# Kernel optimization log

Measured on AMD Instinct MI355X. Metric: run time of the kernel, lower is better.

The kernel has to match this reference:

```python
import jax, jax.numpy as jnp
import numpy as np
from jax.scipy.special import logsumexp

EPSILON = 0.01        # temperature
DIST_THRESH = 0.2
NUM_ITERS = 3
NEG_INF = -1.0e9

B, N, M, C = 4, 4096, 4096, 256


def setup_inputs() -> dict:
    key = jax.random.key(0)
    k1, k2, k3, k4, k5 = jax.random.split(key, 5)
    source_feats = jax.random.normal(k1, (B, N, C), dtype=jnp.float32)
    source_locs = jax.random.uniform(k2, (B, N, 2), dtype=jnp.float32)
    target_locs = jax.random.uniform(k3, (B, M, 2), dtype=jnp.float32)
    source_valid_mask = jax.random.bernoulli(k4, 0.9, (B, N))
    target_valid_mask = jax.random.bernoulli(k5, 0.9, (B, M))
    return {
        "source_feats": source_feats,
        "source_locs": source_locs,
        "target_locs": target_locs,
        "source_valid_mask": source_valid_mask,
        "target_valid_mask": target_valid_mask,
    }


def reference(source_feats, source_locs, target_locs, source_valid_mask, target_valid_mask):
    # pairwise squared distances: [B, M, N]
    diff = target_locs[:, :, None, :] - source_locs[:, None, :, :]  # [B, M, N, 2]
    dist_sq = jnp.sum(diff * diff, axis=-1)                          # [B, M, N]
    log_K = -dist_sq / (EPSILON + 1e-8)

    valid_connection = dist_sq < (DIST_THRESH ** 2)
    valid_connection = valid_connection & source_valid_mask[:, None, :]
    valid_connection = valid_connection & target_valid_mask[:, :, None]
    log_K = jnp.where(valid_connection, log_K, NEG_INF)

    # Sinkhorn iterations in log space
    v = jnp.zeros((log_K.shape[0], 1, log_K.shape[2]), dtype=log_K.dtype)  # [B,1,N]
    u = jnp.zeros((log_K.shape[0], log_K.shape[1], 1), dtype=log_K.dtype)  # [B,M,1]
    for _ in range(NUM_ITERS):
        u = -logsumexp(log_K + v, axis=2, keepdims=True)
        v = -logsumexp(log_K + u, axis=1, keepdims=True)
        v = jnp.where(source_valid_mask[:, None, :], v, 0.0)

    attn = jnp.exp(log_K + u + v)  # [B, M, N]
    attn = jax.lax.stop_gradient(attn)  # original computes it under torch.no_grad

    target_feats = jnp.einsum('bmn,bnc->bmc', attn, source_feats)
    target_feats = target_feats * target_valid_mask[:, :, None].astype(target_feats.dtype)
    has_source = jnp.any(valid_connection, axis=-1, keepdims=True)
    target_feats = target_feats * has_source.astype(target_feats.dtype)
    return target_feats
```

## Files before the change

### kernel.cpp

```cpp
#include <hip/hip_runtime.h>
#include <math.h>

#define BB 4
#define BN 4096
#define CC 256
constexpr float T2      = 0.04f;
constexpr float NEGINF  = -1.0e9f;
constexpr float INV_EPS = (float)(1.0 / 0.01000001);

__device__ __forceinline__ int cell_of(float x, float y) {
  int cx = (int)(x * 5.0f); cx = cx < 0 ? 0 : (cx > 4 ? 4 : cx);
  int cy = (int)(y * 5.0f); cy = cy < 0 ? 0 : (cy > 4 ? 4 : cy);
  return cy * 5 + cx;
}

__global__ void k_count(const float* __restrict__ tlocs, const float* __restrict__ slocs,
                        int* __restrict__ counts_t, int* __restrict__ counts_s) {
  int gid = blockIdx.x * 256 + threadIdx.x;
  if (gid < BB * BN) {
    int b = gid >> 12;
    atomicAdd(&counts_t[b * 32 + cell_of(tlocs[gid * 2], tlocs[gid * 2 + 1])], 1);
  } else {
    int g = gid - BB * BN;
    int b = g >> 12;
    atomicAdd(&counts_s[b * 32 + cell_of(slocs[g * 2], slocs[g * 2 + 1])], 1);
  }
}

__global__ void k_scan_scatter(const float* __restrict__ tlocs, const float* __restrict__ slocs,
                               const int* __restrict__ tmask, const int* __restrict__ smask,
                               const int* __restrict__ counts_t, const int* __restrict__ counts_s,
                               int* __restrict__ starts_t, int* __restrict__ starts_s,
                               int* __restrict__ perm_t, int* __restrict__ perm_s,
                               float4* __restrict__ t_sorted, float4* __restrict__ s_sorted) {
  const int which = blockIdx.x & 1, b = blockIdx.x >> 1;
  const float* locs = which ? slocs : tlocs;
  const int*   mask = which ? smask : tmask;
  const int* counts = which ? counts_s : counts_t;
  int* starts       = which ? starts_s : starts_t;
  int* perm         = which ? perm_s : perm_t;
  float4* pack      = which ? s_sorted : t_sorted;
  __shared__ int st[26];
  __shared__ int cur[25];
  if (threadIdx.x == 0) {
    int acc = 0;
    for (int c = 0; c < 25; c++) { st[c] = acc; acc += counts[b * 32 + c]; }
    st[25] = acc;
  }
  __syncthreads();
  if (threadIdx.x < 25) cur[threadIdx.x] = st[threadIdx.x];
  if (threadIdx.x < 26) starts[b * 32 + threadIdx.x] = st[threadIdx.x];
  __syncthreads();
  for (int i = threadIdx.x; i < BN; i += 256) {
    float x = locs[(b * BN + i) * 2], y = locs[(b * BN + i) * 2 + 1];
    int pos = atomicAdd(&cur[cell_of(x, y)], 1);
    perm[b * BN + pos] = i;
    pack[b * BN + pos] = make_float4(x, y, 0.f, mask[b * BN + i] ? 1.f : 0.f);
  }
}

__global__ __launch_bounds__(256) void k_sink(const float4* __restrict__ opp,
                                              float4* __restrict__ own,
                                              const int* __restrict__ opp_starts,
                                              const int* __restrict__ Zin,
                                              int* __restrict__ Zout,
                                              int zero_invalid) {
  const int row  = blockIdx.x * 4 + (threadIdx.x >> 6);
  const int b    = row >> 12;
  const int lane = threadIdx.x & 63;
  const float4 me = own[row];
  float mrun = -1e30f, srun = 0.f;
  if (me.w != 0.f) {
    const int cell = cell_of(me.x, me.y);
    const int cy = cell / 5, cx = cell % 5;
    const int ry0 = max(cy - 1, 0), ry1 = min(cy + 1, 4);
    const int rx0 = max(cx - 1, 0), rx1 = min(cx + 1, 4);
    for (int ry = ry0; ry <= ry1; ry++) {
      const int r0 = opp_starts[b * 32 + ry * 5 + rx0];
      const int r1 = opp_starts[b * 32 + ry * 5 + rx1 + 1];
      for (int j = r0 + lane; j < r1; j += 64) {
        float4 o = opp[b * BN + j];
        float dx = me.x - o.x, dy = me.y - o.y;
        float d2 = fmaf(dx, dx, dy * dy);
        bool  c  = (d2 < T2) && (o.w != 0.f);
        float t  = c ? fmaf(d2, -INV_EPS, o.z) : -3e30f;
        float d  = t - mrun;
        float e  = __expf(-fabsf(d));
        if (d > 0.f) { srun = fmaf(srun, e, 1.f); mrun = t; }
        else         { srun += e; }
      }
    }
  }
  for (int off = 32; off > 0; off >>= 1) {
    float om = __shfl_down(mrun, off);
    float os = __shfl_down(srun, off);
    float nm = fmaxf(mrun, om);
    srun = srun * __expf(mrun - nm) + os * __expf(om - nm);
    mrun = nm;
  }
  if (lane == 0) {
    const int Z = Zin[b];
    float m0 = mrun, s = srun;
    if (Z > 0) {
      m0 = fmaxf(mrun, 0.f);
      s  = srun * __expf(mrun - m0) + (float)Z * __expf(-m0);
    }
    float val = (s > 0.f) ? -(m0 + logf(s)) : 1.0e9f;
    if (zero_invalid && me.w == 0.f) val = 0.f;
    own[row] = make_float4(me.x, me.y, val, me.w);
    if (val == 1.0e9f) atomicAdd(&Zout[b], 1);
  }
}

#define MAXCH 12

__global__ __launch_bounds__(256) void k_out(
    const float* __restrict__ feats, const float4* __restrict__ t_sorted,
    const float4* __restrict__ s_sorted, const int* __restrict__ perm_t,
    const int* __restrict__ perm_s, const int* __restrict__ starts_t,
    const int* __restrict__ starts_s, float* __restrict__ out) {
  const int b = blockIdx.z;
  const int cell = blockIdx.y / 3, rsel = blockIdx.y % 3;
  const int cy = cell / 5, cx = cell % 5;
  const int ry = cy + rsel - 1;
  if (ry < 0 || ry > 4) return;
  const int t0 = starts_t[b * 32 + cell], t1 = starts_t[b * 32 + cell + 1];
  const int base = t0 + blockIdx.x * 32;
  if (base >= t1) return;
  const int rx0 = max(cx - 1, 0), rx1 = min(cx + 1, 4);
  const int s0 = starts_s[b * 32 + ry * 5 + rx0];
  const int s1 = starts_s[b * 32 + ry * 5 + rx1 + 1];
  if (s0 >= s1) return;
  const int nt = min(32, t1 - base);

  __shared__ float4 tL[32];
  __shared__ int    morg[32];
  __shared__ float4 sL[16];
  __shared__ int    sorg[16];
  __shared__ __align__(16) float attnL[16][32];
  __shared__ __align__(16) float fL[16 * 256];

  const int tid = threadIdx.x;
  if (tid < 32) {
    if (tid < nt) {
      tL[tid]   = t_sorted[b * BN + base + tid];
      morg[tid] = perm_t[b * BN + base + tid];
    } else {
      tL[tid]   = make_float4(0.f, 0.f, 0.f, 0.f);
      morg[tid] = 0;
    }
  }
  const int tmg = tid >> 5;
  const int chg = tid & 31;
  float acc[4][8];
  #pragma unroll
  for (int i = 0; i < 4; i++)
    #pragma unroll
    for (int j = 0; j < 8; j++) acc[i][j] = 0.f;
  __syncthreads();

  for (int n0 = s0; n0 < s1; n0 += 16) {
    const int kk = min(16, s1 - n0);
    __syncthreads();
    if (tid < 16) {
      if (tid < kk) {
        sL[tid]   = s_sorted[b * BN + n0 + tid];
        sorg[tid] = perm_s[b * BN + n0 + tid];
      } else {
        sL[tid]   = make_float4(1e9f, 1e9f, 0.f, 0.f);
        sorg[tid] = 0;
      }
    }
    __syncthreads();
    {
      int e = tid * 2;
      #pragma unroll
      for (int q = 0; q < 2; q++, e++) {
        int nn = e >> 5, tm = e & 31;
        float4 t4 = tL[tm];
        float4 s4 = sL[nn];
        float dx = t4.x - s4.x, dy = t4.y - s4.y;
        float d2 = fmaf(dx, dx, dy * dy);
        bool  c  = (d2 < T2) && (s4.w != 0.f) && (t4.w != 0.f);
        attnL[nn][tm] = c ? __expf(fmaf(d2, -INV_EPS, t4.z + s4.z)) : 0.f;
      }
    }
    #pragma unroll
    for (int q = 0; q < 4; q++) {
      int idx = q * 256 + tid;
      ((float4*)fL)[idx] =
          ((const float4*)feats)[(((b << 12) + sorg[idx >> 6]) << 6) + (idx & 63)];
    }
    __syncthreads();
    #pragma unroll 4
    for (int nn = 0; nn < 16; nn++) {
      const float4 av = *(const float4*)&attnL[nn][tmg * 4];
      const float4 f0 = *(const float4*)&fL[nn * 256 + chg * 4];
      const float4 f1 = *(const float4*)&fL[nn * 256 + 128 + chg * 4];
      float avv[4] = {av.x, av.y, av.z, av.w};
      float ff[8]  = {f0.x, f0.y, f0.z, f0.w, f1.x, f1.y, f1.z, f1.w};
      #pragma unroll
      for (int i = 0; i < 4; i++)
        #pragma unroll
        for (int j = 0; j < 8; j++)
          acc[i][j] = fmaf(avv[i], ff[j], acc[i][j]);
    }
  }
  __syncthreads();
  #pragma unroll
  for (int i = 0; i < 4; i++) {
    int tm = tmg * 4 + i;
    if (tm < nt) {
      float* op = out + (((b << 12) + morg[tm]) << 8) + chg * 4;
      #pragma unroll
      for (int j = 0; j < 4; j++) atomicAdd(op + j,       acc[i][j]);
      #pragma unroll
      for (int j = 0; j < 4; j++) atomicAdd(op + 128 + j, acc[i][j + 4]);
    }
  }
}

extern "C" void kernel_launch(void* const* d_in, const int* in_sizes, int n_in,
                              void* d_out, int out_size, void* d_ws, size_t ws_size,
                              hipStream_t stream) {
  const float* feats = (const float*)d_in[0];
  const float* slocs = (const float*)d_in[1];
  const float* tlocs = (const float*)d_in[2];
  const int*   smask = (const int*)d_in[3];
  const int*   tmask = (const int*)d_in[4];
  float* out = (float*)d_out;

  char* ws = (char*)d_ws;
  int*    counts_t = (int*)(ws);
  int*    counts_s = (int*)(ws + 512);
  int*    Zc       = (int*)(ws + 1024);
  int*    starts_t = (int*)(ws + 2048);
  int*    starts_s = (int*)(ws + 2560);
  int*    perm_t   = (int*)(ws + 4096);
  int*    perm_s   = (int*)(ws + 69632);
  float4* s_sorted = (float4*)(ws + 135168);
  float4* t_sorted = (float4*)(ws + 397312);

  hipMemsetAsync(ws, 0, 2048, stream);
  hipMemsetAsync(out, 0, (size_t)out_size * sizeof(float), stream);
  k_count<<<128, 256, 0, stream>>>(tlocs, slocs, counts_t, counts_s);
  k_scan_scatter<<<8, 256, 0, stream>>>(tlocs, slocs, tmask, smask,
                                        counts_t, counts_s, starts_t, starts_s,
                                        perm_t, perm_s, t_sorted, s_sorted);
  for (int it = 0; it < 3; it++) {
    k_sink<<<4096, 256, 0, stream>>>(s_sorted, t_sorted, starts_s,
                                     Zc + (it == 0 ? 0 : (2 * it) * 4),
                                     Zc + (2 * it + 1) * 4, 0);
    k_sink<<<4096, 256, 0, stream>>>(t_sorted, s_sorted, starts_t,
                                     Zc + (2 * it + 1) * 4,
                                     Zc + (2 * it + 2) * 4, 1);
  }
  k_out<<<dim3(MAXCH, 75, BB), 256, 0, stream>>>(feats, t_sorted, s_sorted,
                                                 perm_t, perm_s, starts_t,
                                                 starts_s, out);
}
```

Before: 604.0 us.

## Fuse Sinkhorn passes into cooperative kernel and drop atomics in output kernel

The six per-half-iteration Sinkhorn launches become one cooperative kernel that loops over phases with grid-wide syncs, removing five launch gaps. The output kernel now lets each block walk all three neighbouring source row bands itself. Each block owns a 128-channel half for its 32 targets, so results are written with plain float4 stores instead of atomics, and the output memset goes away. Source features and attention tiles are double-buffered through registers and shared memory to overlap global loads with the multiply-accumulate. The costs are a reliance on cooperative launch residency (1024 blocks), grid.sync overhead, and serialising over more source chunks per block.

```diff
diff --git a/kernel.cpp b/kernel.cpp
--- a/kernel.cpp
+++ b/kernel.cpp
@@ -1,11 +1,12 @@
 #include <hip/hip_runtime.h>
+#include <hip/hip_cooperative_groups.h>
 #include <math.h>
+
+namespace cg = cooperative_groups;
 
 #define BB 4
 #define BN 4096
-#define CC 256
 constexpr float T2      = 0.04f;
-constexpr float NEGINF  = -1.0e9f;
 constexpr float INV_EPS = (float)(1.0 / 0.01000001);
 
 __device__ __forceinline__ int cell_of(float x, float y) {
@@ -59,88 +60,108 @@
   }
 }
 
-__global__ __launch_bounds__(256) void k_sink(const float4* __restrict__ opp,
-                                              float4* __restrict__ own,
-                                              const int* __restrict__ opp_starts,
-                                              const int* __restrict__ Zin,
-                                              int* __restrict__ Zout,
-                                              int zero_invalid) {
-  const int row  = blockIdx.x * 4 + (threadIdx.x >> 6);
-  const int b    = row >> 12;
+__global__ __launch_bounds__(256) void k_sink_all(
+    float4* __restrict__ t_sorted, float4* __restrict__ s_sorted,
+    const int* __restrict__ starts_t, const int* __restrict__ starts_s,
+    int* __restrict__ Zc) {
+  cg::grid_group grid = cg::this_grid();
+  const int wid  = (blockIdx.x << 2) + (threadIdx.x >> 6);
   const int lane = threadIdx.x & 63;
-  const float4 me = own[row];
-  float mrun = -1e30f, srun = 0.f;
-  if (me.w != 0.f) {
-    const int cell = cell_of(me.x, me.y);
-    const int cy = cell / 5, cx = cell % 5;
-    const int ry0 = max(cy - 1, 0), ry1 = min(cy + 1, 4);
-    const int rx0 = max(cx - 1, 0), rx1 = min(cx + 1, 4);
-    for (int ry = ry0; ry <= ry1; ry++) {
-      const int r0 = opp_starts[b * 32 + ry * 5 + rx0];
-      const int r1 = opp_starts[b * 32 + ry * 5 + rx1 + 1];
-      for (int j = r0 + lane; j < r1; j += 64) {
-        float4 o = opp[b * BN + j];
-        float dx = me.x - o.x, dy = me.y - o.y;
-        float d2 = fmaf(dx, dx, dy * dy);
-        bool  c  = (d2 < T2) && (o.w != 0.f);
-        float t  = c ? fmaf(d2, -INV_EPS, o.z) : -3e30f;
-        float d  = t - mrun;
-        float e  = __expf(-fabsf(d));
-        if (d > 0.f) { srun = fmaf(srun, e, 1.f); mrun = t; }
-        else         { srun += e; }
-      }
-    }
-  }
-  for (int off = 32; off > 0; off >>= 1) {
-    float om = __shfl_down(mrun, off);
-    float os = __shfl_down(srun, off);
-    float nm = fmaxf(mrun, om);
-    srun = srun * __expf(mrun - nm) + os * __expf(om - nm);
-    mrun = nm;
-  }
-  if (lane == 0) {
-    const int Z = Zin[b];
-    float m0 = mrun, s = srun;
-    if (Z > 0) {
-      m0 = fmaxf(mrun, 0.f);
-      s  = srun * __expf(mrun - m0) + (float)Z * __expf(-m0);
-    }
-    float val = (s > 0.f) ? -(m0 + logf(s)) : 1.0e9f;
-    if (zero_invalid && me.w == 0.f) val = 0.f;
-    own[row] = make_float4(me.x, me.y, val, me.w);
-    if (val == 1.0e9f) atomicAdd(&Zout[b], 1);
+  for (int ph = 0; ph < 6; ph++) {
+    float4*       own = (ph & 1) ? s_sorted : t_sorted;
+    const float4* opp = (ph & 1) ? t_sorted : s_sorted;
+    const int*    ost = (ph & 1) ? starts_t : starts_s;
+    const int* Zin = Zc + ph * 4;
+    int*      Zout = Zc + (ph + 1) * 4;
+    const int zero_invalid = (ph & 1);
+    for (int row = wid; row < BB * BN; row += 4096) {
+      const int b = row >> 12;
+      const float4 me = own[row];
+      float mrun = -1e30f, srun = 0.f;
+      if (me.w != 0.f) {
+        const int cell = cell_of(me.x, me.y);
+        const int cy = cell / 5, cx = cell % 5;
+        const int ry0 = max(cy - 1, 0), ry1 = min(cy + 1, 4);
+        const int rx0 = max(cx - 1, 0), rx1 = min(cx + 1, 4);
+        for (int ry = ry0; ry <= ry1; ry++) {
+          const int r0 = ost[b * 32 + ry * 5 + rx0];
+          const int r1 = ost[b * 32 + ry * 5 + rx1 + 1];
+          for (int j = r0 + lane; j < r1; j += 64) {
+            float4 o = opp[b * BN + j];
+            float dx = me.x - o.x, dy = me.y - o.y;
+            float d2 = fmaf(dx, dx, dy * dy);
+            bool  c  = (d2 < T2) && (o.w != 0.f);
+            float t  = c ? fmaf(d2, -INV_EPS, o.z) : -3e30f;
+            float d  = t - mrun;
+            float e  = __expf(-fabsf(d));
+            if (d > 0.f) { srun = fmaf(srun, e, 1.f); mrun = t; }
+            else         { srun += e; }
+          }
+        }
+      }
+      for (int off = 32; off > 0; off >>= 1) {
+        float om = __shfl_down(mrun, off);
+        float os = __shfl_down(srun, off);
+        float nm = fmaxf(mrun, om);
+        srun = srun * __expf(mrun - nm) + os * __expf(om - nm);
+        mrun = nm;
+      }
+      if (lane == 0) {
+        const int Z = Zin[b];
+        float m0 = mrun, s = srun;
+        if (Z > 0) {
+          m0 = fmaxf(mrun, 0.f);
+          s  = srun * __expf(mrun - m0) + (float)Z * __expf(-m0);
+        }
+        float val = (s > 0.f) ? -(m0 + logf(s)) : 1.0e9f;
+        if (zero_invalid && me.w == 0.f) val = 0.f;
+        own[row] = make_float4(me.x, me.y, val, me.w);
+        if (val == 1.0e9f) atomicAdd(&Zout[b], 1);
+      }
+    }
+    grid.sync();
   }
 }
 
 #define MAXCH 12
 
 __global__ __launch_bounds__(256) void k_out(
-    const float* __restrict__ feats, const float4* __restrict__ t_sorted,
+    const float4* __restrict__ featsF4, const float4* __restrict__ t_sorted,
     const float4* __restrict__ s_sorted, const int* __restrict__ perm_t,
     const int* __restrict__ perm_s, const int* __restrict__ starts_t,
-    const int* __restrict__ starts_s, float* __restrict__ out) {
-  const int b = blockIdx.z;
-  const int cell = blockIdx.y / 3, rsel = blockIdx.y % 3;
-  const int cy = cell / 5, cx = cell % 5;
-  const int ry = cy + rsel - 1;
-  if (ry < 0 || ry > 4) return;
+    const int* __restrict__ starts_s, float4* __restrict__ outF4) {
+  const int b    = blockIdx.z >> 1;
+  const int chO  = (blockIdx.z & 1) << 5;
+  const int cell = blockIdx.y;
   const int t0 = starts_t[b * 32 + cell], t1 = starts_t[b * 32 + cell + 1];
   const int base = t0 + blockIdx.x * 32;
   if (base >= t1) return;
+  const int nt = min(32, t1 - base);
+
+  const int cy = cell / 5, cx = cell % 5;
   const int rx0 = max(cx - 1, 0), rx1 = min(cx + 1, 4);
-  const int s0 = starts_s[b * 32 + ry * 5 + rx0];
-  const int s1 = starts_s[b * 32 + ry * 5 + rx1 + 1];
-  if (s0 >= s1) return;
-  const int nt = min(32, t1 - base);
+  int r0[3], len[3];
+  #pragma unroll
+  for (int k = 0; k < 3; k++) {
+    int ry = cy + k - 1;
+    if (ry >= 0 && ry <= 4) {
+      int a = starts_s[b * 32 + ry * 5 + rx0];
+      int e = starts_s[b * 32 + ry * 5 + rx1 + 1];
+      r0[k] = a; len[k] = e - a;
+    } else { r0[k] = 0; len[k] = 0; }
+  }
+  const int total   = len[0] + len[1] + len[2];
+  const int nchunks = (total + 15) >> 4;
 
   __shared__ float4 tL[32];
   __shared__ int    morg[32];
-  __shared__ float4 sL[16];
-  __shared__ int    sorg[16];
-  __shared__ __align__(16) float attnL[16][32];
-  __shared__ __align__(16) float fL[16 * 256];
-
-  const int tid = threadIdx.x;
+  __shared__ __align__(16) float  attnL[2][16][32];
+  __shared__ __align__(16) float4 fL[2][512];
+
+  const int tid  = threadIdx.x;
+  const int w    = tid >> 6, lane = tid & 63;
+  const int tmg  = tid >> 5, chg = tid & 31;
+
   if (tid < 32) {
     if (tid < nt) {
       tL[tid]   = t_sorted[b * BN + base + tid];
@@ -150,72 +171,112 @@
       morg[tid] = 0;
     }
   }
-  const int tmg = tid >> 5;
-  const int chg = tid & 31;
-  float acc[4][8];
+
+  float acc[4][4];
   #pragma unroll
   for (int i = 0; i < 4; i++)
     #pragma unroll
-    for (int j = 0; j < 8; j++) acc[i][j] = 0.f;
+    for (int j = 0; j < 4; j++) acc[i][j] = 0.f;
+
+  float4 sreg = make_float4(1e9f, 1e9f, 0.f, 0.f);
+  int    sorgreg = 0;
+  auto loadS = [&](int chunk) {
+    int v  = chunk * 16 + lane;
+    int jj = -1;
+    if (v < len[0]) jj = r0[0] + v;
+    else {
+      v -= len[0];
+      if (v < len[1]) jj = r0[1] + v;
+      else {
+        v -= len[1];
+        if (v < len[2]) jj = r0[2] + v;
+      }
+    }
+    if (lane < 16) {
+      if (jj >= 0) {
+        sreg    = s_sorted[b * BN + jj];
+        sorgreg = perm_s[b * BN + jj];
+      } else {
+        sreg    = make_float4(1e9f, 1e9f, 0.f, 0.f);
+        sorgreg = 0;
+      }
+    }
+  };
+  float4 greg[2];
+  auto issue_loads = [&]() {
+    #pragma unroll
+    for (int q = 0; q < 2; q++) {
+      int row = (w << 2) + (q << 1) + (lane >> 5);
+      int so  = __shfl(sorgreg, row);
+      greg[q] = featsF4[(((b << 12) + so) << 6) + chO + (lane & 31)];
+    }
+  };
+  auto write_fl = [&](int bi) {
+    #pragma unroll
+    for (int q = 0; q < 2; q++)
+      fL[bi][(w << 7) + (q << 6) + lane] = greg[q];
+  };
+  auto stage_attn = [&](int bi) {
+    #pragma unroll
+    for (int q = 0; q < 2; q++) {
+      int e  = tid * 2 + q;
+      int nn = e >> 5, tm = e & 31;
+      float sx = __shfl(sreg.x, nn);
+      float sy = __shfl(sreg.y, nn);
+      float sv = __shfl(sreg.z, nn);
+      float sw = __shfl(sreg.w, nn);
+      float4 t4 = tL[tm];
+      float dx = t4.x - sx, dy = t4.y - sy;
+      float d2 = fmaf(dx, dx, dy * dy);
+      bool  c  = (d2 < T2) && (sw != 0.f) && (t4.w != 0.f);
+      attnL[bi][nn][tm] = c ? __expf(fmaf(d2, -INV_EPS, t4.z + sv)) : 0.f;
+    }
+  };
+  auto mac = [&](int bi) {
+    #pragma unroll
+    for (int nn = 0; nn < 16; nn++) {
+      const float4 av = *(const float4*)&attnL[bi][nn][tmg << 2];
+      const float4 f  = fL[bi][(nn << 5) + chg];
+      #pragma unroll
+      for (int i = 0; i < 4; i++) {
+        float a = (&av.x)[i];
+        acc[i][0] = fmaf(a, f.x, acc[i][0]);
+        acc[i][1] = fmaf(a, f.y, acc[i][1]);
+        acc[i][2] = fmaf(a, f.z, acc[i][2]);
+        acc[i][3] = fmaf(a, f.w, acc[i][3]);
+      }
+    }
+  };
+
+  loadS(0);
   __syncthreads();
-
-  for (int n0 = s0; n0 < s1; n0 += 16) {
-    const int kk = min(16, s1 - n0);
+  if (nchunks > 0) {
+    issue_loads();
+    write_fl(0);
+    stage_attn(0);
+    loadS(1);
+  }
+  __syncthreads();
+
+  for (int i = 0; i < nchunks; i++) {
+    const int cur = i & 1, nxt = cur ^ 1;
+    const bool more = (i + 1) < nchunks;
+    if (more) issue_loads();
+    mac(cur);
+    if (more) {
+      write_fl(nxt);
+      stage_attn(nxt);
+      loadS(i + 2);
+    }
     __syncthreads();
-    if (tid < 16) {
-      if (tid < kk) {
-        sL[tid]   = s_sorted[b * BN + n0 + tid];
-        sorg[tid] = perm_s[b * BN + n0 + tid];
-      } else {
-        sL[tid]   = make_float4(1e9f, 1e9f, 0.f, 0.f);
-        sorg[tid] = 0;
-      }
-    }
-    __syncthreads();
-    {
-      int e = tid * 2;
-      #pragma unroll
-      for (int q = 0; q < 2; q++, e++) {
-        int nn = e >> 5, tm = e & 31;
-        float4 t4 = tL[tm];
-        float4 s4 = sL[nn];
-        float dx = t4.x - s4.x, dy = t4.y - s4.y;
-        float d2 = fmaf(dx, dx, dy * dy);
-        bool  c  = (d2 < T2) && (s4.w != 0.f) && (t4.w != 0.f);
-        attnL[nn][tm] = c ? __expf(fmaf(d2, -INV_EPS, t4.z + s4.z)) : 0.f;
-      }
-    }
-    #pragma unroll
-    for (int q = 0; q < 4; q++) {
-      int idx = q * 256 + tid;
-      ((float4*)fL)[idx] =
-          ((const float4*)feats)[(((b << 12) + sorg[idx >> 6]) << 6) + (idx & 63)];
-    }
-    __syncthreads();
-    #pragma unroll 4
-    for (int nn = 0; nn < 16; nn++) {
-      const float4 av = *(const float4*)&attnL[nn][tmg * 4];
-      const float4 f0 = *(const float4*)&fL[nn * 256 + chg * 4];
-      const float4 f1 = *(const float4*)&fL[nn * 256 + 128 + chg * 4];
-      float avv[4] = {av.x, av.y, av.z, av.w};
-      float ff[8]  = {f0.x, f0.y, f0.z, f0.w, f1.x, f1.y, f1.z, f1.w};
-      #pragma unroll
-      for (int i = 0; i < 4; i++)
-        #pragma unroll
-        for (int j = 0; j < 8; j++)
-          acc[i][j] = fmaf(avv[i], ff[j], acc[i][j]);
-    }
-  }
-  __syncthreads();
+  }
+
   #pragma unroll
   for (int i = 0; i < 4; i++) {
-    int tm = tmg * 4 + i;
+    int tm = (tmg << 2) + i;
     if (tm < nt) {
-      float* op = out + (((b << 12) + morg[tm]) << 8) + chg * 4;
-      #pragma unroll
-      for (int j = 0; j < 4; j++) atomicAdd(op + j,       acc[i][j]);
-      #pragma unroll
-      for (int j = 0; j < 4; j++) atomicAdd(op + 128 + j, acc[i][j + 4]);
+      outF4[(((b << 12) + morg[tm]) << 6) + chO + chg] =
+          make_float4(acc[i][0], acc[i][1], acc[i][2], acc[i][3]);
     }
   }
 }
@@ -228,7 +289,6 @@
   const float* tlocs = (const float*)d_in[2];
   const int*   smask = (const int*)d_in[3];
   const int*   tmask = (const int*)d_in[4];
-  float* out = (float*)d_out;
 
   char* ws = (char*)d_ws;
   int*    counts_t = (int*)(ws);
@@ -242,20 +302,13 @@
   float4* t_sorted = (float4*)(ws + 397312);
 
   hipMemsetAsync(ws, 0, 2048, stream);
-  hipMemsetAsync(out, 0, (size_t)out_size * sizeof(float), stream);
   k_count<<<128, 256, 0, stream>>>(tlocs, slocs, counts_t, counts_s);
   k_scan_scatter<<<8, 256, 0, stream>>>(tlocs, slocs, tmask, smask,
                                         counts_t, counts_s, starts_t, starts_s,
                                         perm_t, perm_s, t_sorted, s_sorted);
-  for (int it = 0; it < 3; it++) {
-    k_sink<<<4096, 256, 0, stream>>>(s_sorted, t_sorted, starts_s,
-                                     Zc + (it == 0 ? 0 : (2 * it) * 4),
-                                     Zc + (2 * it + 1) * 4, 0);
-    k_sink<<<4096, 256, 0, stream>>>(t_sorted, s_sorted, starts_t,
-                                     Zc + (2 * it + 1) * 4,
-                                     Zc + (2 * it + 2) * 4, 1);
-  }
-  k_out<<<dim3(MAXCH, 75, BB), 256, 0, stream>>>(feats, t_sorted, s_sorted,
-                                                 perm_t, perm_s, starts_t,
-                                                 starts_s, out);
-}
+  void* args[] = {&t_sorted, &s_sorted, &starts_t, &starts_s, &Zc};
+  hipLaunchCooperativeKernel((void*)k_sink_all, dim3(1024), dim3(256), args, 0, stream);
+  k_out<<<dim3(MAXCH, 25, BB * 2), 256, 0, stream>>>(
+      (const float4*)feats, t_sorted, s_sorted, perm_t, perm_s,
+      starts_t, starts_s, (float4*)d_out);
+}
```

After: 1.594 ms. 2.64x slower.

## Unroll sinkhorn loads and restructure output kernel with channel split and double buffering

Applied to the files above, without the earlier changes.

The sinkhorn row kernel now issues four neighbor loads per lane before computing, so more memory requests are in flight at once. The output kernel splits the 256 channels into two halves across extra blocks, which doubles the grid and halves each thread's accumulators. It reads features straight from global memory into registers instead of staging them in shared memory. It also double-buffers the source metadata and attention tile, cutting one barrier per chunk. The cost is that neighbor positions and attention weights are recomputed for each channel half, and more atomic-add blocks write to the output.

```diff
diff --git a/kernel.cpp b/kernel.cpp
--- a/kernel.cpp
+++ b/kernel.cpp
@@ -3,9 +3,7 @@
 
 #define BB 4
 #define BN 4096
-#define CC 256
 constexpr float T2      = 0.04f;
-constexpr float NEGINF  = -1.0e9f;
 constexpr float INV_EPS = (float)(1.0 / 0.01000001);
 
 __device__ __forceinline__ int cell_of(float x, float y) {
@@ -59,6 +57,7 @@
   }
 }
 
+#define UNR 4
 __global__ __launch_bounds__(256) void k_sink(const float4* __restrict__ opp,
                                               float4* __restrict__ own,
                                               const int* __restrict__ opp_starts,
@@ -75,19 +74,28 @@
     const int cy = cell / 5, cx = cell % 5;
     const int ry0 = max(cy - 1, 0), ry1 = min(cy + 1, 4);
     const int rx0 = max(cx - 1, 0), rx1 = min(cx + 1, 4);
+    const float4* oppB = opp + b * BN;
     for (int ry = ry0; ry <= ry1; ry++) {
       const int r0 = opp_starts[b * 32 + ry * 5 + rx0];
       const int r1 = opp_starts[b * 32 + ry * 5 + rx1 + 1];
-      for (int j = r0 + lane; j < r1; j += 64) {
-        float4 o = opp[b * BN + j];
-        float dx = me.x - o.x, dy = me.y - o.y;
-        float d2 = fmaf(dx, dx, dy * dy);
-        bool  c  = (d2 < T2) && (o.w != 0.f);
-        float t  = c ? fmaf(d2, -INV_EPS, o.z) : -3e30f;
-        float d  = t - mrun;
-        float e  = __expf(-fabsf(d));
-        if (d > 0.f) { srun = fmaf(srun, e, 1.f); mrun = t; }
-        else         { srun += e; }
+      for (int base = r0 + lane; base < r1; base += 64 * UNR) {
+        float4 buf[UNR];
+        #pragma unroll
+        for (int u = 0; u < UNR; u++)
+          buf[u] = oppB[base + u * 64];
+        #pragma unroll
+        for (int u = 0; u < UNR; u++) {
+          const int j = base + u * 64;
+          float4 o = buf[u];
+          float dx = me.x - o.x, dy = me.y - o.y;
+          float d2 = fmaf(dx, dx, dy * dy);
+          bool  c  = (j < r1) && (d2 < T2) && (o.w != 0.f);
+          float t  = c ? fmaf(d2, -INV_EPS, o.z) : -3e30f;
+          float d  = t - mrun;
+          float e  = __expf(-fabsf(d));
+          if (d > 0.f) { srun = fmaf(srun, e, 1.f); mrun = t; }
+          else         { srun += e; }
+        }
       }
     }
   }
@@ -115,14 +123,17 @@
 #define MAXCH 12
 
 __global__ __launch_bounds__(256) void k_out(
-    const float* __restrict__ feats, const float4* __restrict__ t_sorted,
+    const float4* __restrict__ featsF4, const float4* __restrict__ t_sorted,
     const float4* __restrict__ s_sorted, const int* __restrict__ perm_t,
     const int* __restrict__ perm_s, const int* __restrict__ starts_t,
     const int* __restrict__ starts_s, float* __restrict__ out) {
-  const int b = blockIdx.z;
-  const int cell = blockIdx.y / 3, rsel = blockIdx.y % 3;
+  const int z    = blockIdx.z;
+  const int b    = z / 6;
+  const int rp   = (z % 6) >> 1;
+  const int chO  = (z & 1) << 5;
+  const int cell = blockIdx.y;
   const int cy = cell / 5, cx = cell % 5;
-  const int ry = cy + rsel - 1;
+  const int ry = cy + rp - 1;
   if (ry < 0 || ry > 4) return;
   const int t0 = starts_t[b * 32 + cell], t1 = starts_t[b * 32 + cell + 1];
   const int base = t0 + blockIdx.x * 32;
@@ -131,16 +142,18 @@
   const int s0 = starts_s[b * 32 + ry * 5 + rx0];
   const int s1 = starts_s[b * 32 + ry * 5 + rx1 + 1];
   if (s0 >= s1) return;
-  const int nt = min(32, t1 - base);
+  const int nt      = min(32, t1 - base);
+  const int nchunks = (s1 - s0 + 15) >> 4;
 
   __shared__ float4 tL[32];
   __shared__ int    morg[32];
-  __shared__ float4 sL[16];
-  __shared__ int    sorg[16];
-  __shared__ __align__(16) float attnL[16][32];
-  __shared__ __align__(16) float fL[16 * 256];
+  __shared__ float4 sL[2][16];
+  __shared__ int    sorgL[2][16];
+  __shared__ __align__(16) float attnF[512];
 
   const int tid = threadIdx.x;
+  const int tmg = tid >> 5, chg = tid & 31;
+
   if (tid < 32) {
     if (tid < nt) {
       tL[tid]   = t_sorted[b * BN + base + tid];
@@ -150,72 +163,100 @@
       morg[tid] = 0;
     }
   }
-  const int tmg = tid >> 5;
-  const int chg = tid & 31;
-  float acc[4][8];
+  if (tid < 16) {
+    int j = s0 + tid;
+    if (j < s1) {
+      sL[0][tid]    = s_sorted[b * BN + j];
+      sorgL[0][tid] = perm_s[b * BN + j];
+    } else {
+      sL[0][tid]    = make_float4(1e9f, 1e9f, 0.f, 0.f);
+      sorgL[0][tid] = 0;
+    }
+  }
+  __syncthreads();
+  {
+    float2 a2;
+    #pragma unroll
+    for (int q = 0; q < 2; q++) {
+      int e = tid * 2 + q, nn = e >> 5, tm = e & 31;
+      float4 t4 = tL[tm];
+      float4 s4 = sL[0][nn];
+      float dx = t4.x - s4.x, dy = t4.y - s4.y;
+      float d2 = fmaf(dx, dx, dy * dy);
+      bool  c  = (d2 < T2) && (s4.w != 0.f) && (t4.w != 0.f);
+      (&a2.x)[q] = c ? __expf(fmaf(d2, -INV_EPS, t4.z + s4.z)) : 0.f;
+    }
+    ((float2*)attnF)[tid] = a2;
+  }
+  __syncthreads();
+
+  float acc[4][4];
   #pragma unroll
   for (int i = 0; i < 4; i++)
     #pragma unroll
-    for (int j = 0; j < 8; j++) acc[i][j] = 0.f;
-  __syncthreads();
-
-  for (int n0 = s0; n0 < s1; n0 += 16) {
-    const int kk = min(16, s1 - n0);
+    for (int j = 0; j < 4; j++) acc[i][j] = 0.f;
+
+  const int fbase = (b << 12) << 6;
+  for (int i = 0; i < nchunks; i++) {
+    const int cur = i & 1, nxt = cur ^ 1;
+    const bool more = (i + 1) < nchunks;
+    if (more && tid < 16) {
+      int j = s0 + (i + 1) * 16 + tid;
+      if (j < s1) {
+        sL[nxt][tid]    = s_sorted[b * BN + j];
+        sorgL[nxt][tid] = perm_s[b * BN + j];
+      } else {
+        sL[nxt][tid]    = make_float4(1e9f, 1e9f, 0.f, 0.f);
+        sorgL[nxt][tid] = 0;
+      }
+    }
+    #pragma unroll
+    for (int g = 0; g < 4; g++) {
+      float4 fr[4];
+      #pragma unroll
+      for (int q = 0; q < 4; q++) {
+        int so = sorgL[cur][g * 4 + q];
+        fr[q] = featsF4[fbase + (so << 6) + chO + chg];
+      }
+      #pragma unroll
+      for (int q = 0; q < 4; q++) {
+        const int nn = g * 4 + q;
+        const float4 av = *(const float4*)&attnF[(nn << 5) + (tmg << 2)];
+        #pragma unroll
+        for (int ii = 0; ii < 4; ii++) {
+          float a = (&av.x)[ii];
+          acc[ii][0] = fmaf(a, fr[q].x, acc[ii][0]);
+          acc[ii][1] = fmaf(a, fr[q].y, acc[ii][1]);
+          acc[ii][2] = fmaf(a, fr[q].z, acc[ii][2]);
+          acc[ii][3] = fmaf(a, fr[q].w, acc[ii][3]);
+        }
+      }
+    }
     __syncthreads();
-    if (tid < 16) {
-      if (tid < kk) {
-        sL[tid]   = s_sorted[b * BN + n0 + tid];
-        sorg[tid] = perm_s[b * BN + n0 + tid];
-      } else {
-        sL[tid]   = make_float4(1e9f, 1e9f, 0.f, 0.f);
-        sorg[tid] = 0;
-      }
-    }
-    __syncthreads();
-    {
-      int e = tid * 2;
+    if (more) {
+      float2 a2;
       #pragma unroll
-      for (int q = 0; q < 2; q++, e++) {
-        int nn = e >> 5, tm = e & 31;
+      for (int q = 0; q < 2; q++) {
+        int e = tid * 2 + q, nn = e >> 5, tm = e & 31;
         float4 t4 = tL[tm];
-        float4 s4 = sL[nn];
+        float4 s4 = sL[nxt][nn];
         float dx = t4.x - s4.x, dy = t4.y - s4.y;
         float d2 = fmaf(dx, dx, dy * dy);
         bool  c  = (d2 < T2) && (s4.w != 0.f) && (t4.w != 0.f);
-        attnL[nn][tm] = c ? __expf(fmaf(d2, -INV_EPS, t4.z + s4.z)) : 0.f;
-      }
-    }
-    #pragma unroll
-    for (int q = 0; q < 4; q++) {
-      int idx = q * 256 + tid;
-      ((float4*)fL)[idx] =
-          ((const float4*)feats)[(((b << 12) + sorg[idx >> 6]) << 6) + (idx & 63)];
+        (&a2.x)[q] = c ? __expf(fmaf(d2, -INV_EPS, t4.z + s4.z)) : 0.f;
+      }
+      ((float2*)attnF)[tid] = a2;
     }
     __syncthreads();
-    #pragma unroll 4
-    for (int nn = 0; nn < 16; nn++) {
-      const float4 av = *(const float4*)&attnL[nn][tmg * 4];
-      const float4 f0 = *(const float4*)&fL[nn * 256 + chg * 4];
-      const float4 f1 = *(const float4*)&fL[nn * 256 + 128 + chg * 4];
-      float avv[4] = {av.x, av.y, av.z, av.w};
-      float ff[8]  = {f0.x, f0.y, f0.z, f0.w, f1.x, f1.y, f1.z, f1.w};
-      #pragma unroll
-      for (int i = 0; i < 4; i++)
-        #pragma unroll
-        for (int j = 0; j < 8; j++)
-          acc[i][j] = fmaf(avv[i], ff[j], acc[i][j]);
-    }
-  }
-  __syncthreads();
+  }
+
   #pragma unroll
   for (int i = 0; i < 4; i++) {
-    int tm = tmg * 4 + i;
+    int tm = (tmg << 2) + i;
     if (tm < nt) {
-      float* op = out + (((b << 12) + morg[tm]) << 8) + chg * 4;
+      float* op = out + (((b << 12) + morg[tm]) << 8) + (chO << 2) + (chg << 2);
       #pragma unroll
-      for (int j = 0; j < 4; j++) atomicAdd(op + j,       acc[i][j]);
-      #pragma unroll
-      for (int j = 0; j < 4; j++) atomicAdd(op + 128 + j, acc[i][j + 4]);
+      for (int j = 0; j < 4; j++) atomicAdd(op + j, acc[i][j]);
     }
   }
 }
@@ -255,7 +296,7 @@
                                      Zc + (2 * it + 1) * 4,
                                      Zc + (2 * it + 2) * 4, 1);
   }
-  k_out<<<dim3(MAXCH, 75, BB), 256, 0, stream>>>(feats, t_sorted, s_sorted,
-                                                 perm_t, perm_s, starts_t,
-                                                 starts_s, out);
-}
+  k_out<<<dim3(MAXCH, 25, BB * 6), 256, 0, stream>>>(
+      (const float4*)feats, t_sorted, s_sorted, perm_t, perm_s,
+      starts_t, starts_s, out);
+}
```

Result: slower. 784.5 us (+29.9%).
